# Kernel optimization log

Hardware: AMD Instinct MI355X
Metric: run time of the kernel (lower is better)

## Reference

```python
import jax, jax.numpy as jnp
import numpy as np

S, B, IN, H = 512, 128, 256, 512  # seq_len, batch, input_size, hidden_size


def setup_inputs() -> dict:
    key = jax.random.key(0)
    ks = jax.random.split(key, 17)
    def p(k, shape):
        return jax.random.normal(k, shape, dtype=jnp.float32) * 0.05
    inp = {
        "x": jax.random.normal(ks[0], (S, B, IN), dtype=jnp.float32),
        "h0": jnp.zeros((1, B, H), dtype=jnp.float32),
        "c0": jnp.zeros((1, B, H), dtype=jnp.float32),
    }
    # gates: f=forget, i=input, o=output, g=cell candidate
    for j, n in enumerate(["f", "i", "o", "g"]):
        inp[f"W{n}"] = p(ks[1 + 4 * j], (H, IN))
        inp[f"bW{n}"] = p(ks[2 + 4 * j], (H,))
        inp[f"U{n}"] = p(ks[3 + 4 * j], (H, H))
        inp[f"bU{n}"] = p(ks[4 + 4 * j], (H,))
    return inp


def reference(x, h0, c0, Wf, bWf, Uf, bUf, Wi, bWi, Ui, bUi,
              Wo, bWo, Uo, bUo, Wg, bWg, Ug, bUg):
    # Fuse the 4 input projections and 4 recurrent projections into single GEMMs.
    # Math is identical to applying each Linear separately.
    Wcat = jnp.concatenate([Wf, Wi, Wo, Wg], axis=0)      # [4H, IN]
    bcat = jnp.concatenate([bWf + bUf, bWi + bUi, bWo + bUo, bWg + bUg])  # [4H]
    Ucat = jnp.concatenate([Uf, Ui, Uo, Ug], axis=0)      # [4H, H]
    hd = h0.shape[-1]
    # Precompute input-dependent gate pre-activations for all timesteps.
    xg = jnp.einsum('sbi,gi->sbg', x, Wcat) + bcat        # [S, B, 4H]

    def step(carry, xg_t):
        h, c = carry
        g = xg_t + h @ Ucat.T                             # [B, 4H]
        f = jax.nn.sigmoid(g[..., :hd])
        i = jax.nn.sigmoid(g[..., hd:2 * hd])
        o = jax.nn.sigmoid(g[..., 2 * hd:3 * hd])
        cand = jnp.tanh(g[..., 3 * hd:])
        c = f * c + i * cand
        h = o * jnp.tanh(c)
        return (h, c), h

    (h, c), h_seq = jax.lax.scan(step, (h0[-1], c0[-1]), xg)
    return h_seq, h, c
```

## Files before the change

### kernel.cpp

```cpp
#include <hip/hip_runtime.h>
#include <hip/hip_cooperative_groups.h>

namespace cg = cooperative_groups;


#define SQ   512
#define BB   128
#define IN_  256
#define HH   512
#define RG   8
#define CGN  16
#define RINGHALF (BB * HH)
#define RING_OFF 1024

typedef float    f32x4 __attribute__((ext_vector_type(4)));
typedef short    s16x8 __attribute__((ext_vector_type(8)));
typedef unsigned u32x4 __attribute__((ext_vector_type(4)));

struct P {
  const float *x, *h0, *c0;
  const float *W[4], *bW[4], *U[4], *bU[4];
  float* out;
  unsigned* ring;
  int mode;
};

__device__ __forceinline__ unsigned f2b(float f) {
  unsigned u = __float_as_uint(f);
  return (u + 0x7FFFu + ((u >> 16) & 1u)) >> 16;
}
__device__ __forceinline__ float sigm(float x) { return 1.f / (1.f + __expf(-x)); }
__device__ __forceinline__ float tanh_(float x) {
  float e = __expf(-2.f * fabsf(x));
  float t = (1.f - e) / (1.f + e);
  return copysignf(t, x);
}
__device__ __forceinline__ u32x4 pack8(f32x4 a, f32x4 b) {
  u32x4 d;
  d.x = f2b(a.x) | (f2b(a.y) << 16);
  d.y = f2b(a.z) | (f2b(a.w) << 16);
  d.z = f2b(b.x) | (f2b(b.y) << 16);
  d.w = f2b(b.z) | (f2b(b.w) << 16);
  return d;
}

#define LOAD4_LLC(c0_,c1_,c2_,c3_,ptr_)                                      \
  asm volatile(                                                              \
    "global_load_dwordx4 %0, %4, off sc0 sc1\n\t"                            \
    "global_load_dwordx4 %1, %4, off offset:16 sc0 sc1\n\t"                  \
    "global_load_dwordx4 %2, %4, off offset:32 sc0 sc1\n\t"                  \
    "global_load_dwordx4 %3, %4, off offset:48 sc0 sc1\n\t"                  \
    "s_waitcnt vmcnt(0)"                                                     \
    : "=&v"(c0_), "=&v"(c1_), "=&v"(c2_), "=&v"(c3_)                         \
    : "v"(ptr_) : "memory")

__global__ void __launch_bounds__(512, 1) lstm_all(P p) {
  __shared__ unsigned short Hs[16][512];
  __shared__ unsigned short Xs[2][16][256];
  __shared__ float gbuf[4][16][33];

  const int tid = threadIdx.x;
  const int bid = blockIdx.x;
  const int r   = bid & 7;
  const int cgi = bid >> 3;
  const int rb  = r * 16;
  const int hcb = cgi * 32;

  const int w8   = tid >> 6;
  const int gate = w8 >> 1;
  const int ct   = w8 & 1;
  const int l    = tid & 63;
  const int l16  = l & 15;
  const int lk   = l >> 4;
  const int srow = tid >> 5;
  const int sn   = tid & 31;

  unsigned* ring = p.ring;

  const int colb = hcb + ct * 16 + l16;
  const float* Wg = p.W[gate];
  const float* Ug = p.U[gate];
  s16x8 bfrag[24];
#pragma unroll
  for (int kk = 0; kk < 24; ++kk) {
    int k = kk * 32 + lk * 8;
    const float* src = (kk < 8) ? (Wg + (size_t)colb * IN_ + k)
                                : (Ug + (size_t)colb * HH + (k - IN_));
    f32x4 a = *(const f32x4*)src;
    f32x4 b = *(const f32x4*)(src + 4);
    s16x8 v;
    v[0]=(short)f2b(a.x); v[1]=(short)f2b(a.y); v[2]=(short)f2b(a.z); v[3]=(short)f2b(a.w);
    v[4]=(short)f2b(b.x); v[5]=(short)f2b(b.y); v[6]=(short)f2b(b.z); v[7]=(short)f2b(b.w);
    bfrag[kk] = v;
  }
  const float bias = p.bW[gate][colb] + p.bU[gate][colb];
  float cval = p.c0[(size_t)(rb + srow) * HH + hcb + sn];

  const int wswz = (srow & 7) << 4;
  const int rswz = (l16 & 7) << 4;
  char* HsB = (char*)&Hs[0][0];
  char* XsB = (char*)&Xs[0][0][0];

  f32x4 xg0, xg1;
  {
    const float* xs = p.x + (size_t)(rb + srow) * IN_ + sn * 8;
    xg0 = *(const f32x4*)(xs);
    xg1 = *(const f32x4*)(xs + 4);
  }

  for (int t = 0; t < SQ; ++t) {
    {
      char* xrow = XsB + (t & 1) * 8192 + srow * 512;
      *(u32x4*)(xrow + ((sn * 16) ^ wswz)) = pack8(xg0, xg1);
      if (t + 1 < SQ) {
        const float* xs = p.x + ((size_t)(t + 1) * BB + rb + srow) * IN_ + sn * 8;
        xg0 = *(const f32x4*)(xs);
        xg1 = *(const f32x4*)(xs + 4);
      }
    }

    char* hrow = HsB + srow * 1024;
    if (t == 0) {
      const float* hs = p.h0 + (size_t)(rb + srow) * HH + sn * 16;
      f32x4 a0 = *(const f32x4*)(hs);
      f32x4 b0 = *(const f32x4*)(hs + 4);
      f32x4 a1 = *(const f32x4*)(hs + 8);
      f32x4 b1 = *(const f32x4*)(hs + 12);
      *(u32x4*)(hrow + ((sn * 32)      ^ wswz)) = pack8(a0, b0);
      *(u32x4*)(hrow + ((sn * 32 + 16) ^ wswz)) = pack8(a1, b1);
    } else if (p.mode == 0) {
      const unsigned* hb = ring + (((t - 1) & 1) ? RINGHALF : 0)
                         + (size_t)(rb + srow) * HH + sn * 16;
      u32x4 c0, c1, c2, c3;
      const unsigned tg = (unsigned)t;
#define TAGOK(v) (((v).x >> 16) == tg && ((v).y >> 16) == tg && \
                  ((v).z >> 16) == tg && ((v).w >> 16) == tg)
      int spin = 0;
      for (;;) {
        LOAD4_LLC(c0, c1, c2, c3, hb);
        if (TAGOK(c0) && TAGOK(c1) && TAGOK(c2) && TAGOK(c3)) break;
        if (++spin > (1 << 16)) break;
        if (spin > 8) __builtin_amdgcn_s_sleep(1);
      }
#undef TAGOK
      u32x4 w0, w1;
      w0.x = (c0.x & 0xFFFFu) | (c0.y << 16);
      w0.y = (c0.z & 0xFFFFu) | (c0.w << 16);
      w0.z = (c1.x & 0xFFFFu) | (c1.y << 16);
      w0.w = (c1.z & 0xFFFFu) | (c1.w << 16);
      w1.x = (c2.x & 0xFFFFu) | (c2.y << 16);
      w1.y = (c2.z & 0xFFFFu) | (c2.w << 16);
      w1.z = (c3.x & 0xFFFFu) | (c3.y << 16);
      w1.w = (c3.z & 0xFFFFu) | (c3.w << 16);
      *(u32x4*)(hrow + ((sn * 32)      ^ wswz)) = w0;
      *(u32x4*)(hrow + ((sn * 32 + 16) ^ wswz)) = w1;
    } else {
      cg::this_grid().sync();
      const float* hp = p.out + ((size_t)(t - 1) * BB + rb + srow) * HH + sn * 16;
      u32x4 a0, a1, a2, a3;
      LOAD4_LLC(a0, a1, a2, a3, hp);
      f32x4 f0 = __builtin_bit_cast(f32x4, a0);
      f32x4 f1 = __builtin_bit_cast(f32x4, a1);
      f32x4 f2 = __builtin_bit_cast(f32x4, a2);
      f32x4 f3 = __builtin_bit_cast(f32x4, a3);
      *(u32x4*)(hrow + ((sn * 32)      ^ wswz)) = pack8(f0, f1);
      *(u32x4*)(hrow + ((sn * 32 + 16) ^ wswz)) = pack8(f2, f3);
    }
    __syncthreads();

    f32x4 acc0 = { bias, bias, bias, bias };
    f32x4 acc1 = { 0.f, 0.f, 0.f, 0.f };
    const char* xr = XsB + (t & 1) * 8192 + l16 * 512;
    const char* hr = HsB + l16 * 1024;
#pragma unroll
    for (int kp = 0; kp < 8; kp += 2) {
      s16x8 a0 = *(const s16x8*)(xr + ((kp * 64 + lk * 16)       ^ rswz));
      s16x8 a1 = *(const s16x8*)(xr + (((kp + 1) * 64 + lk * 16) ^ rswz));
      acc0 = __builtin_amdgcn_mfma_f32_16x16x32_bf16(a0, bfrag[kp],     acc0, 0, 0, 0);
      acc1 = __builtin_amdgcn_mfma_f32_16x16x32_bf16(a1, bfrag[kp + 1], acc1, 0, 0, 0);
    }
#pragma unroll
    for (int kp = 0; kp < 16; kp += 2) {
      s16x8 a0 = *(const s16x8*)(hr + ((kp * 64 + lk * 16)       ^ rswz));
      s16x8 a1 = *(const s16x8*)(hr + (((kp + 1) * 64 + lk * 16) ^ rswz));
      acc0 = __builtin_amdgcn_mfma_f32_16x16x32_bf16(a0, bfrag[8 + kp], acc0, 0, 0, 0);
      acc1 = __builtin_amdgcn_mfma_f32_16x16x32_bf16(a1, bfrag[9 + kp], acc1, 0, 0, 0);
    }

#pragma unroll
    for (int rr = 0; rr < 4; ++rr) {
      float v = acc0[rr] + acc1[rr];
      v = (gate < 3) ? sigm(v) : tanh_(v);
      gbuf[gate][lk * 4 + rr][ct * 16 + l16] = v;
    }
    __syncthreads();

    float f = gbuf[0][srow][sn];
    float i = gbuf[1][srow][sn];
    float o = gbuf[2][srow][sn];
    float g = gbuf[3][srow][sn];
    cval = f * cval + i * g;
    float h = o * tanh_(cval);

    size_t oidx = ((size_t)t * BB + rb + srow) * HH + hcb + sn;
    if (p.mode == 0) {
      unsigned tw = ((unsigned)(t + 1) << 16) | f2b(h);
      unsigned* dst = ring + ((t & 1) ? RINGHALF : 0)
                    + (size_t)(rb + srow) * HH + hcb + sn;
      asm volatile("global_store_dword %0, %1, off sc0 sc1"
                   :: "v"(dst), "v"(tw) : "memory");
      __builtin_nontemporal_store(h, p.out + oidx);
    } else {
      asm volatile("global_store_dword %0, %1, off sc0 sc1"
                   :: "v"(p.out + oidx), "v"(h) : "memory");
      asm volatile("s_waitcnt vmcnt(0)" ::: "memory");
    }
    if (t == SQ - 1) {
      size_t base = (size_t)SQ * BB * HH;
      size_t idx2 = (size_t)(rb + srow) * HH + hcb + sn;
      p.out[base + idx2] = h;
      p.out[base + (size_t)BB * HH + idx2] = cval;
    }
  }
}

extern "C" void kernel_launch(void* const* d_in, const int* in_sizes, int n_in,
                              void* d_out, int out_size, void* d_ws, size_t ws_size,
                              hipStream_t stream) {
  P p;
  p.x  = (const float*)d_in[0];
  p.h0 = (const float*)d_in[1];
  p.c0 = (const float*)d_in[2];
  for (int g = 0; g < 4; ++g) {
    p.W[g]  = (const float*)d_in[3 + 4 * g];
    p.bW[g] = (const float*)d_in[4 + 4 * g];
    p.U[g]  = (const float*)d_in[5 + 4 * g];
    p.bU[g] = (const float*)d_in[6 + 4 * g];
  }
  p.out = (float*)d_out;

  const size_t need = (size_t)(RING_OFF + 2 * BB * HH) * sizeof(unsigned);
  const bool ws_ok = (d_ws != nullptr) && (ws_size >= need);
  p.mode = ws_ok ? 0 : 2;
  p.ring = ws_ok ? ((unsigned*)d_ws + RING_OFF) : nullptr;
  if (ws_ok) hipMemsetAsync(d_ws, 0, need, stream);

  void* args[] = { &p };
  hipError_t e = hipLaunchCooperativeKernel((const void*)lstm_all,
                                            dim3(RG * CGN), dim3(512),
                                            args, 0, stream);
  if (e != hipSuccess) {
    hipLaunchKernelGGL(lstm_all, dim3(RG * CGN), dim3(512), 0, stream, p);
  }
}
```

Measured before the change: 1.479 ms.

## Double block count by splitting K across waves and narrowing hidden tiles

```diff
diff --git a/kernel.cpp b/kernel.cpp
--- a/kernel.cpp
+++ b/kernel.cpp
@@ -9,7 +9,7 @@
 #define IN_  256
 #define HH   512
 #define RG   8
-#define CGN  16
+#define CGN  32
 #define RINGHALF (BB * HH)
 #define RING_OFF 1024
 
@@ -35,21 +35,27 @@
   float t = (1.f - e) / (1.f + e);
   return copysignf(t, x);
 }
+__device__ __forceinline__ unsigned cvtpk(float lo, float hi) {
+  unsigned r;
+  asm("v_cvt_pk_bf16_f32 %0, %1, %2" : "=v"(r) : "v"(lo), "v"(hi));
+  return r;
+}
 __device__ __forceinline__ u32x4 pack8(f32x4 a, f32x4 b) {
   u32x4 d;
-  d.x = f2b(a.x) | (f2b(a.y) << 16);
-  d.y = f2b(a.z) | (f2b(a.w) << 16);
-  d.z = f2b(b.x) | (f2b(b.y) << 16);
-  d.w = f2b(b.z) | (f2b(b.w) << 16);
+  d.x = cvtpk(a.x, a.y); d.y = cvtpk(a.z, a.w);
+  d.z = cvtpk(b.x, b.y); d.w = cvtpk(b.z, b.w);
   return d;
 }
-
-#define LOAD4_LLC(c0_,c1_,c2_,c3_,ptr_)                                      \
+__device__ __forceinline__ unsigned mergelo(unsigned d0, unsigned d1) {
+  return __builtin_amdgcn_perm(d1, d0, 0x05040100u);
+}
+
+#define LOAD4S_LLC(c0_,c1_,c2_,c3_,ptr_)                                     \
   asm volatile(                                                              \
     "global_load_dwordx4 %0, %4, off sc0 sc1\n\t"                            \
-    "global_load_dwordx4 %1, %4, off offset:16 sc0 sc1\n\t"                  \
-    "global_load_dwordx4 %2, %4, off offset:32 sc0 sc1\n\t"                  \
-    "global_load_dwordx4 %3, %4, off offset:48 sc0 sc1\n\t"                  \
+    "global_load_dwordx4 %1, %4, off offset:512 sc0 sc1\n\t"                 \
+    "global_load_dwordx4 %2, %4, off offset:1024 sc0 sc1\n\t"                \
+    "global_load_dwordx4 %3, %4, off offset:1536 sc0 sc1\n\t"                \
     "s_waitcnt vmcnt(0)"                                                     \
     : "=&v"(c0_), "=&v"(c1_), "=&v"(c2_), "=&v"(c3_)                         \
     : "v"(ptr_) : "memory")
@@ -57,35 +63,35 @@
 __global__ void __launch_bounds__(512, 1) lstm_all(P p) {
   __shared__ unsigned short Hs[16][512];
   __shared__ unsigned short Xs[2][16][256];
-  __shared__ float gbuf[4][16][33];
+  __shared__ float pbuf[2][4][16][17];
 
   const int tid = threadIdx.x;
   const int bid = blockIdx.x;
   const int r   = bid & 7;
   const int cgi = bid >> 3;
   const int rb  = r * 16;
-  const int hcb = cgi * 32;
-
-  const int w8   = tid >> 6;
-  const int gate = w8 >> 1;
-  const int ct   = w8 & 1;
-  const int l    = tid & 63;
-  const int l16  = l & 15;
-  const int lk   = l >> 4;
-  const int srow = tid >> 5;
-  const int sn   = tid & 31;
+  const int hcb = cgi * 16;
+
+  const int w8    = tid >> 6;
+  const int gate  = w8 & 3;
+  const int khalf = w8 >> 2;
+  const int l     = tid & 63;
+  const int l16   = l & 15;
+  const int lk    = l >> 4;
+  const int srow  = tid >> 5;
+  const int sn    = tid & 31;
 
   unsigned* ring = p.ring;
 
-  const int colb = hcb + ct * 16 + l16;
+  const int col = hcb + l16;
   const float* Wg = p.W[gate];
   const float* Ug = p.U[gate];
-  s16x8 bfrag[24];
-#pragma unroll
-  for (int kk = 0; kk < 24; ++kk) {
-    int k = kk * 32 + lk * 8;
-    const float* src = (kk < 8) ? (Wg + (size_t)colb * IN_ + k)
-                                : (Ug + (size_t)colb * HH + (k - IN_));
+  s16x8 bfrag[12];
+#pragma unroll
+  for (int kk = 0; kk < 12; ++kk) {
+    int K = (khalf * 12 + kk) * 32 + lk * 8;
+    const float* src = (K < IN_) ? (Wg + (size_t)col * IN_ + K)
+                                 : (Ug + (size_t)col * HH + (K - IN_));
     f32x4 a = *(const f32x4*)src;
     f32x4 b = *(const f32x4*)(src + 4);
     s16x8 v;
@@ -93,8 +99,11 @@
     v[4]=(short)f2b(b.x); v[5]=(short)f2b(b.y); v[6]=(short)f2b(b.z); v[7]=(short)f2b(b.w);
     bfrag[kk] = v;
   }
-  const float bias = p.bW[gate][colb] + p.bU[gate][colb];
-  float cval = p.c0[(size_t)(rb + srow) * HH + hcb + sn];
+  const float bias = (khalf == 0) ? (p.bW[gate][col] + p.bU[gate][col]) : 0.f;
+
+  float cval = 0.f;
+  if (tid < 256)
+    cval = p.c0[(size_t)(rb + (tid >> 4)) * HH + hcb + (tid & 15)];
 
   const int wswz = (srow & 7) << 4;
   const int rswz = (l16 & 7) << 4;
@@ -121,50 +130,50 @@
 
     char* hrow = HsB + srow * 1024;
     if (t == 0) {
-      const float* hs = p.h0 + (size_t)(rb + srow) * HH + sn * 16;
-      f32x4 a0 = *(const f32x4*)(hs);
-      f32x4 b0 = *(const f32x4*)(hs + 4);
-      f32x4 a1 = *(const f32x4*)(hs + 8);
-      f32x4 b1 = *(const f32x4*)(hs + 12);
-      *(u32x4*)(hrow + ((sn * 32)      ^ wswz)) = pack8(a0, b0);
-      *(u32x4*)(hrow + ((sn * 32 + 16) ^ wswz)) = pack8(a1, b1);
+      const float* hs = p.h0 + (size_t)(rb + srow) * HH + sn * 4;
+#pragma unroll
+      for (int cc = 0; cc < 4; ++cc) {
+        f32x4 v = *(const f32x4*)(hs + cc * 128);
+        uint2 u = make_uint2(cvtpk(v.x, v.y), cvtpk(v.z, v.w));
+        *(uint2*)(hrow + ((sn * 8 + cc * 256) ^ wswz)) = u;
+      }
     } else if (p.mode == 0) {
       const unsigned* hb = ring + (((t - 1) & 1) ? RINGHALF : 0)
-                         + (size_t)(rb + srow) * HH + sn * 16;
+                         + (size_t)(rb + srow) * HH + sn * 4;
       u32x4 c0, c1, c2, c3;
-      const unsigned tg = (unsigned)t;
-#define TAGOK(v) (((v).x >> 16) == tg && ((v).y >> 16) == tg && \
-                  ((v).z >> 16) == tg && ((v).w >> 16) == tg)
+      const unsigned tgw = (unsigned)t << 16;
       int spin = 0;
       for (;;) {
-        LOAD4_LLC(c0, c1, c2, c3, hb);
-        if (TAGOK(c0) && TAGOK(c1) && TAGOK(c2) && TAGOK(c3)) break;
+        LOAD4S_LLC(c0, c1, c2, c3, hb);
+        unsigned m = (c0.x^tgw)|(c0.y^tgw)|(c0.z^tgw)|(c0.w^tgw)
+                   | (c1.x^tgw)|(c1.y^tgw)|(c1.z^tgw)|(c1.w^tgw)
+                   | (c2.x^tgw)|(c2.y^tgw)|(c2.z^tgw)|(c2.w^tgw)
+                   | (c3.x^tgw)|(c3.y^tgw)|(c3.z^tgw)|(c3.w^tgw);
+        if ((m & 0xFFFF0000u) == 0u) break;
         if (++spin > (1 << 16)) break;
         if (spin > 8) __builtin_amdgcn_s_sleep(1);
       }
-#undef TAGOK
-      u32x4 w0, w1;
-      w0.x = (c0.x & 0xFFFFu) | (c0.y << 16);
-      w0.y = (c0.z & 0xFFFFu) | (c0.w << 16);
-      w0.z = (c1.x & 0xFFFFu) | (c1.y << 16);
-      w0.w = (c1.z & 0xFFFFu) | (c1.w << 16);
-      w1.x = (c2.x & 0xFFFFu) | (c2.y << 16);
-      w1.y = (c2.z & 0xFFFFu) | (c2.w << 16);
-      w1.z = (c3.x & 0xFFFFu) | (c3.y << 16);
-      w1.w = (c3.z & 0xFFFFu) | (c3.w << 16);
-      *(u32x4*)(hrow + ((sn * 32)      ^ wswz)) = w0;
-      *(u32x4*)(hrow + ((sn * 32 + 16) ^ wswz)) = w1;
+      *(uint2*)(hrow + ((sn * 8)       ^ wswz)) =
+          make_uint2(mergelo(c0.x, c0.y), mergelo(c0.z, c0.w));
+      *(uint2*)(hrow + ((sn * 8 + 256) ^ wswz)) =
+          make_uint2(mergelo(c1.x, c1.y), mergelo(c1.z, c1.w));
+      *(uint2*)(hrow + ((sn * 8 + 512) ^ wswz)) =
+          make_uint2(mergelo(c2.x, c2.y), mergelo(c2.z, c2.w));
+      *(uint2*)(hrow + ((sn * 8 + 768) ^ wswz)) =
+          make_uint2(mergelo(c3.x, c3.y), mergelo(c3.z, c3.w));
     } else {
       cg::this_grid().sync();
-      const float* hp = p.out + ((size_t)(t - 1) * BB + rb + srow) * HH + sn * 16;
+      const float* hp = p.out + ((size_t)(t - 1) * BB + rb + srow) * HH + sn * 4;
       u32x4 a0, a1, a2, a3;
-      LOAD4_LLC(a0, a1, a2, a3, hp);
+      LOAD4S_LLC(a0, a1, a2, a3, hp);
       f32x4 f0 = __builtin_bit_cast(f32x4, a0);
       f32x4 f1 = __builtin_bit_cast(f32x4, a1);
       f32x4 f2 = __builtin_bit_cast(f32x4, a2);
       f32x4 f3 = __builtin_bit_cast(f32x4, a3);
-      *(u32x4*)(hrow + ((sn * 32)      ^ wswz)) = pack8(f0, f1);
-      *(u32x4*)(hrow + ((sn * 32 + 16) ^ wswz)) = pack8(f2, f3);
+      *(uint2*)(hrow + ((sn * 8)       ^ wswz)) = make_uint2(cvtpk(f0.x,f0.y), cvtpk(f0.z,f0.w));
+      *(uint2*)(hrow + ((sn * 8 + 256) ^ wswz)) = make_uint2(cvtpk(f1.x,f1.y), cvtpk(f1.z,f1.w));
+      *(uint2*)(hrow + ((sn * 8 + 512) ^ wswz)) = make_uint2(cvtpk(f2.x,f2.y), cvtpk(f2.z,f2.w));
+      *(uint2*)(hrow + ((sn * 8 + 768) ^ wswz)) = make_uint2(cvtpk(f3.x,f3.y), cvtpk(f3.z,f3.w));
     }
     __syncthreads();
 
@@ -173,53 +182,53 @@
     const char* xr = XsB + (t & 1) * 8192 + l16 * 512;
     const char* hr = HsB + l16 * 1024;
 #pragma unroll
-    for (int kp = 0; kp < 8; kp += 2) {
-      s16x8 a0 = *(const s16x8*)(xr + ((kp * 64 + lk * 16)       ^ rswz));
-      s16x8 a1 = *(const s16x8*)(xr + (((kp + 1) * 64 + lk * 16) ^ rswz));
-      acc0 = __builtin_amdgcn_mfma_f32_16x16x32_bf16(a0, bfrag[kp],     acc0, 0, 0, 0);
-      acc1 = __builtin_amdgcn_mfma_f32_16x16x32_bf16(a1, bfrag[kp + 1], acc1, 0, 0, 0);
-    }
-#pragma unroll
-    for (int kp = 0; kp < 16; kp += 2) {
-      s16x8 a0 = *(const s16x8*)(hr + ((kp * 64 + lk * 16)       ^ rswz));
-      s16x8 a1 = *(const s16x8*)(hr + (((kp + 1) * 64 + lk * 16) ^ rswz));
-      acc0 = __builtin_amdgcn_mfma_f32_16x16x32_bf16(a0, bfrag[8 + kp], acc0, 0, 0, 0);
-      acc1 = __builtin_amdgcn_mfma_f32_16x16x32_bf16(a1, bfrag[9 + kp], acc1, 0, 0, 0);
-    }
-
-#pragma unroll
-    for (int rr = 0; rr < 4; ++rr) {
-      float v = acc0[rr] + acc1[rr];
-      v = (gate < 3) ? sigm(v) : tanh_(v);
-      gbuf[gate][lk * 4 + rr][ct * 16 + l16] = v;
-    }
+    for (int kk = 0; kk < 12; kk += 2) {
+      int K32a = khalf * 12 + kk;
+      int K32b = K32a + 1;
+      const char* pa = (K32a < 8) ? (xr + ((K32a * 64 + lk * 16) ^ rswz))
+                                  : (hr + (((K32a - 8) * 64 + lk * 16) ^ rswz));
+      const char* pb = (K32b < 8) ? (xr + ((K32b * 64 + lk * 16) ^ rswz))
+                                  : (hr + (((K32b - 8) * 64 + lk * 16) ^ rswz));
+      s16x8 a0 = *(const s16x8*)pa;
+      s16x8 a1 = *(const s16x8*)pb;
+      acc0 = __builtin_amdgcn_mfma_f32_16x16x32_bf16(a0, bfrag[kk],     acc0, 0, 0, 0);
+      acc1 = __builtin_amdgcn_mfma_f32_16x16x32_bf16(a1, bfrag[kk + 1], acc1, 0, 0, 0);
+    }
+
+#pragma unroll
+    for (int rr = 0; rr < 4; ++rr)
+      pbuf[khalf][gate][lk * 4 + rr][l16] = acc0[rr] + acc1[rr];
     __syncthreads();
 
-    float f = gbuf[0][srow][sn];
-    float i = gbuf[1][srow][sn];
-    float o = gbuf[2][srow][sn];
-    float g = gbuf[3][srow][sn];
-    cval = f * cval + i * g;
-    float h = o * tanh_(cval);
-
-    size_t oidx = ((size_t)t * BB + rb + srow) * HH + hcb + sn;
-    if (p.mode == 0) {
-      unsigned tw = ((unsigned)(t + 1) << 16) | f2b(h);
-      unsigned* dst = ring + ((t & 1) ? RINGHALF : 0)
-                    + (size_t)(rb + srow) * HH + hcb + sn;
-      asm volatile("global_store_dword %0, %1, off sc0 sc1"
-                   :: "v"(dst), "v"(tw) : "memory");
-      __builtin_nontemporal_store(h, p.out + oidx);
-    } else {
-      asm volatile("global_store_dword %0, %1, off sc0 sc1"
-                   :: "v"(p.out + oidx), "v"(h) : "memory");
-      asm volatile("s_waitcnt vmcnt(0)" ::: "memory");
-    }
-    if (t == SQ - 1) {
-      size_t base = (size_t)SQ * BB * HH;
-      size_t idx2 = (size_t)(rb + srow) * HH + hcb + sn;
-      p.out[base + idx2] = h;
-      p.out[base + (size_t)BB * HH + idx2] = cval;
+    if (tid < 256) {
+      const int fr = tid >> 4;
+      const int fc = tid & 15;
+      float f = sigm (pbuf[0][0][fr][fc] + pbuf[1][0][fr][fc]);
+      float i = sigm (pbuf[0][1][fr][fc] + pbuf[1][1][fr][fc]);
+      float o = sigm (pbuf[0][2][fr][fc] + pbuf[1][2][fr][fc]);
+      float g = tanh_(pbuf[0][3][fr][fc] + pbuf[1][3][fr][fc]);
+      cval = f * cval + i * g;
+      float h = o * tanh_(cval);
+
+      size_t oidx = ((size_t)t * BB + rb + fr) * HH + hcb + fc;
+      if (p.mode == 0) {
+        unsigned tw = ((unsigned)(t + 1) << 16) | f2b(h);
+        unsigned* dst = ring + ((t & 1) ? RINGHALF : 0)
+                      + (size_t)(rb + fr) * HH + hcb + fc;
+        asm volatile("global_store_dword %0, %1, off sc0 sc1"
+                     :: "v"(dst), "v"(tw) : "memory");
+        __builtin_nontemporal_store(h, p.out + oidx);
+      } else {
+        asm volatile("global_store_dword %0, %1, off sc0 sc1"
+                     :: "v"(p.out + oidx), "v"(h) : "memory");
+        asm volatile("s_waitcnt vmcnt(0)" ::: "memory");
+      }
+      if (t == SQ - 1) {
+        size_t base = (size_t)SQ * BB * HH;
+        size_t idx2 = (size_t)(rb + fr) * HH + hcb + fc;
+        p.out[base + idx2] = h;
+        p.out[base + (size_t)BB * HH + idx2] = cval;
+      }
     }
   }
 }
```

After: 1.709 ms. 15.6% more time.
